# Kernel tuning notes

Hardware: AMD Instinct MI355X
Metric: run time of the kernel (lower is better)

Reference implementation:

```python
import jax, jax.numpy as jnp
import numpy as np

D_MODEL = 1024
N_HEADS = 16
K_TOP = 64
D_HEAD = D_MODEL // N_HEADS


def setup_inputs() -> dict:
    key = jax.random.key(0)
    ks = jax.random.split(key, 9)
    B, L = 8, 4096
    bound = 1.0 / np.sqrt(D_MODEL)  # nn.Linear default init range
    lin = lambda k: jax.random.uniform(k, (D_MODEL, D_MODEL), jnp.float32, -bound, bound)
    vec = lambda k: jax.random.uniform(k, (D_MODEL,), jnp.float32, -bound, bound)
    return {
        "query": jax.random.normal(ks[0], (B, L, D_MODEL), jnp.float32),
        "Wq": lin(ks[1]), "bq": vec(ks[2]),
        "Wk": lin(ks[3]), "bk": vec(ks[4]),
        "Wv": lin(ks[5]), "bv": vec(ks[6]),
        "Wo": lin(ks[7]), "bo": vec(ks[8]),
    }


def reference(query, Wq, bq, Wk, bk, Wv, bv, Wo, bo):
    B, L_q, D = query.shape
    L_k = L_q  # self-attention: key = value = query
    F_q = L_q // 2 + 1
    F_k = L_k // 2 + 1
    k_top = min(K_TOP, F_q)

    def proj(x, W, b):
        # (B, L, D) -> (B, H, L, d_head)
        return (x @ W + b).reshape(B, -1, N_HEADS, D_HEAD).transpose(0, 2, 1, 3)

    q = proj(query, Wq, bq)
    k = proj(query, Wk, bk)
    v = proj(query, Wv, bv)

    q_freq = jnp.fft.rfft(q, axis=2)  # (B, H, F_q, d_head) complex64
    k_freq = jnp.fft.rfft(k, axis=2)
    v_freq = jnp.fft.rfft(v, axis=2)

    # top-k frequency bins by mean spectral magnitude of the query
    q_energy = jnp.abs(q_freq).mean(axis=-1)  # (B, H, F_q)
    _, idx = jax.lax.top_k(q_energy, k_top)   # (B, H, k)
    mapped_idx = jnp.clip(
        jnp.round(idx.astype(jnp.float32) * (F_k - 1) / (F_q - 1)).astype(jnp.int32),
        0, F_k - 1)

    gather = lambda x, i: jnp.take_along_axis(x, i[..., None], axis=2)
    q_top = gather(q_freq, idx)          # (B, H, k, d_head)
    k_top_freq = gather(k_freq, mapped_idx)
    v_top = gather(v_freq, mapped_idx)

    eps = 1e-8
    attn_score = (q_top.real * k_top_freq.real).sum(-1) / (D_HEAD ** 0.5 + eps)
    attn = jax.nn.softmax(attn_score, axis=-1)[..., None]  # (B, H, k, 1)

    # fill spectrum with mean of query spectrum, then scatter attended bins
    q_mean_freq = q_freq.mean(axis=2, keepdims=True)  # (B, H, 1, d_head) complex
    out_freq = jnp.broadcast_to(q_mean_freq, (B, N_HEADS, F_q, D_HEAD))
    src = (attn * v_top.real).astype(out_freq.dtype)  # real -> complex (imag=0)
    bi = jnp.arange(B)[:, None, None]
    hi = jnp.arange(N_HEADS)[None, :, None]
    out_freq = out_freq.at[bi, hi, idx].set(src)

    out_time = jnp.fft.irfft(out_freq, n=L_q, axis=2)  # (B, H, L, d_head)
    out = out_time.transpose(0, 2, 1, 3).reshape(B, L_q, D)
    return out @ Wo + bo
```

## Files before the change

kernel.cpp:

```cpp
#include <hip/hip_runtime.h>
#include <math.h>
#include <stdint.h>


typedef _Float16 f16;
typedef _Float16 f16x8 __attribute__((ext_vector_type(8)));
typedef float f32x4 __attribute__((ext_vector_type(4)));

#define PI_F 3.14159265358979323846f
#define PADJ(j) ((j) + ((j) >> 3))

__device__ __forceinline__ void gl_lds16(const void* g, void* l) {
  __builtin_amdgcn_global_load_lds((const __attribute__((address_space(1))) void*)g,
                                   (__attribute__((address_space(3))) void*)l, 16, 0, 0);
}

__device__ __forceinline__ float2 cadd(float2 a, float2 b) { return make_float2(a.x + b.x, a.y + b.y); }
__device__ __forceinline__ float2 csub(float2 a, float2 b) { return make_float2(a.x - b.x, a.y - b.y); }
__device__ __forceinline__ float2 cmul(float2 a, float2 b) {
  return make_float2(a.x * b.x - a.y * b.y, a.x * b.y + a.y * b.x);
}
__device__ __forceinline__ float2 cmni(float2 a) { return make_float2(a.y, -a.x); }

__global__ __launch_bounds__(256) void k_tw(float2* __restrict__ twtab, float2* __restrict__ utab) {
  int j = blockIdx.x * 256 + threadIdx.x;
  if (j < 2048) {
    float ang = (float)j * (-6.28318530717958647692f / 2048.0f);
    twtab[j] = make_float2(cosf(ang), sinf(ang));
  } else if (j < 4097) {
    int f = j - 2048;
    float ang = (float)f * (-6.28318530717958647692f / 4096.0f);
    utab[f] = make_float2(cosf(ang), sinf(ang));
  }
}

__global__ __launch_bounds__(256) void k_prep(const float* __restrict__ Wq, const float* __restrict__ Wo,
                                              f16* __restrict__ WqT, f16* __restrict__ WoT) {
  __shared__ float t[32][33];
  const float* src = blockIdx.z ? Wo : Wq;
  f16* dst = blockIdx.z ? WoT : WqT;
  int c0 = blockIdx.x * 32, r0 = blockIdx.y * 32;
  int tx = threadIdx.x, ty = threadIdx.y;
#pragma unroll
  for (int yy = 0; yy < 4; ++yy)
    t[ty + yy * 8][tx] = src[(size_t)(r0 + ty + yy * 8) * 1024 + c0 + tx];
  __syncthreads();
#pragma unroll
  for (int yy = 0; yy < 4; ++yy)
    dst[(size_t)(c0 + ty + yy * 8) * 1024 + r0 + tx] = (f16)t[tx][ty + yy * 8];
}

__global__ __launch_bounds__(256) void k_prep2(const float* __restrict__ Wk, const float* __restrict__ Wv,
                                               f16* __restrict__ WkT, f16* __restrict__ WvT) {
  __shared__ float t[32][33];
  const float* src = blockIdx.z ? Wv : Wk;
  f16* dst = blockIdx.z ? WvT : WkT;
  int c0 = blockIdx.x * 32, r0 = blockIdx.y * 32;
  int tx = threadIdx.x, ty = threadIdx.y;
#pragma unroll
  for (int yy = 0; yy < 4; ++yy)
    t[ty + yy * 8][tx] = src[(size_t)(r0 + ty + yy * 8) * 1024 + c0 + tx];
  __syncthreads();
#pragma unroll
  for (int yy = 0; yy < 4; ++yy)
    dst[(size_t)(c0 + ty + yy * 8) * 1024 + r0 + tx] = (f16)t[tx][ty + yy * 8];
}

__global__ __launch_bounds__(256) void k_t1(const float* __restrict__ X, float* __restrict__ Xt) {
  __shared__ float t[32][33];
  int b = blockIdx.z;
  int l0 = blockIdx.x * 32, d0 = blockIdx.y * 32;
  int tx = threadIdx.x, ty = threadIdx.y;
#pragma unroll
  for (int yy = 0; yy < 4; ++yy)
    t[ty + yy * 8][tx] = X[((size_t)b * 4096 + l0 + ty + yy * 8) * 1024 + d0 + tx];
  __syncthreads();
#pragma unroll
  for (int yy = 0; yy < 4; ++yy)
    Xt[((size_t)b * 1024 + d0 + ty + yy * 8) * 4096 + l0 + tx] = t[tx][ty + yy * 8];
}

__device__ __forceinline__ void r8_stage(const float2* __restrict__ cur, float2* __restrict__ nxt,
                                         const float2* __restrict__ tw, int tid, int lg) {
  int Ls = 1 << lg;
  int p = tid >> lg, q = tid & (Ls - 1);
  float2 x[8];
#pragma unroll
  for (int u = 0; u < 8; ++u) x[u] = cur[PADJ(tid + 256 * u)];
  float2 s0 = cadd(x[0], x[4]), d0v = csub(x[0], x[4]);
  float2 s1 = cadd(x[2], x[6]), d1v = csub(x[2], x[6]);
  float2 e0 = cadd(s0, s1), e2 = csub(s0, s1);
  float2 md1 = cmni(d1v);
  float2 e1 = cadd(d0v, md1), e3 = csub(d0v, md1);
  float2 t0 = cadd(x[1], x[5]), u0 = csub(x[1], x[5]);
  float2 t1 = cadd(x[3], x[7]), u1 = csub(x[3], x[7]);
  float2 o0 = cadd(t0, t1), o2 = csub(t0, t1);
  float2 mu1 = cmni(u1);
  float2 o1 = cadd(u0, mu1), o3 = csub(u0, mu1);
  const float C8 = 0.70710678118654752440f;
  float2 w1 = make_float2(C8 * (o1.x + o1.y), C8 * (o1.y - o1.x));
  float2 w2 = cmni(o2);
  float2 w3 = make_float2(C8 * (o3.y - o3.x), -C8 * (o3.x + o3.y));
  float2 y[8];
  y[0] = cadd(e0, o0); y[4] = csub(e0, o0);
  y[1] = cadd(e1, w1); y[5] = csub(e1, w1);
  y[2] = cadd(e2, w2); y[6] = csub(e2, w2);
  y[3] = cadd(e3, w3); y[7] = csub(e3, w3);
  int tb = p << lg;
#pragma unroll
  for (int v = 1; v < 8; ++v) y[v] = cmul(y[v], tw[tb * v]);
  int ob = q + (p << (lg + 3));
#pragma unroll
  for (int v = 0; v < 8; ++v) nxt[PADJ(ob + (v << lg))] = y[v];
}

__global__ __launch_bounds__(256) void k_fft(const float* __restrict__ Xt,
                                             const float2* __restrict__ twtab,
                                             const float2* __restrict__ utab,
                                             f16* __restrict__ PReU, f16* __restrict__ PImU,
                                             float* __restrict__ sumXf) {
  __shared__ float2 bufA[2304];
  __shared__ float2 bufB[2304];
  __shared__ float redr[256], redi[256];
  int tid = threadIdx.x;
  int blk = blockIdx.x;

  const float4* src = (const float4*)(Xt + (size_t)blk * 4096);
#pragma unroll
  for (int r = 0; r < 4; ++r) {
    int i4 = r * 256 + tid;
    float4 v = src[i4];
    bufA[PADJ(2 * i4)] = make_float2(v.x, v.y);
    bufA[PADJ(2 * i4 + 1)] = make_float2(v.z, v.w);
  }
  __syncthreads();
  r8_stage(bufA, bufB, twtab, tid, 0);
  __syncthreads();
  r8_stage(bufB, bufA, twtab, tid, 3);
  __syncthreads();
  r8_stage(bufA, bufB, twtab, tid, 6);
  __syncthreads();
#pragma unroll
  for (int h = 0; h < 2; ++h) {
    int i = (h << 8) + tid;
    float2 a0 = bufB[PADJ(i)], a1 = bufB[PADJ(i + 512)];
    float2 a2 = bufB[PADJ(i + 1024)], a3 = bufB[PADJ(i + 1536)];
    float2 s02 = cadd(a0, a2), d02 = csub(a0, a2);
    float2 s13 = cadd(a1, a3), d13m = cmni(csub(a1, a3));
    bufA[PADJ(i)] = cadd(s02, s13);
    bufA[PADJ(i + 512)] = cadd(d02, d13m);
    bufA[PADJ(i + 1024)] = csub(s02, s13);
    bufA[PADJ(i + 1536)] = csub(d02, d13m);
  }
  __syncthreads();
  float sumr = 0.f, sumi = 0.f;
  size_t obase = (size_t)blk * 2049;
  for (int f = tid; f <= 2048; f += 256) {
    int fz = f & 2047, fm = (2048 - f) & 2047;
    float2 z = bufA[PADJ(fz)], m = bufA[PADJ(fm)];
    float Er = 0.5f * (z.x + m.x), Ei = 0.5f * (z.y - m.y);
    float Or = 0.5f * (z.y + m.y), Oi = -0.5f * (z.x - m.x);
    float2 wv = utab[f];
    float Xr = Er + wv.x * Or - wv.y * Oi;
    float Xi = Ei + wv.x * Oi + wv.y * Or;
    PReU[obase + f] = (f16)Xr;
    PImU[obase + f] = (f16)Xi;
    sumr += Xr; sumi += Xi;
  }
  __syncthreads();
  redr[tid] = sumr; redi[tid] = sumi;
  __syncthreads();
  for (int s = 128; s > 0; s >>= 1) {
    if (tid < s) { redr[tid] += redr[tid + s]; redi[tid] += redi[tid + s]; }
    __syncthreads();
  }
  if (tid == 0) { sumXf[2 * blk] = redr[0]; sumXf[2 * blk + 1] = redi[0]; }
}

__global__ __launch_bounds__(256) void k_C(const float* __restrict__ sumXf, const float* __restrict__ Wq,
                                           const float* __restrict__ bq,
                                           float* __restrict__ Cre, float* __restrict__ Cim) {
  int b = blockIdx.x >> 2;
  int hd = ((blockIdx.x & 3) << 8) + threadIdx.x;
  float accr = 0.f, acci = 0.f;
  for (int dm = 0; dm < 1024; ++dm) {
    float w = Wq[(size_t)dm * 1024 + hd];
    accr += sumXf[2 * (b * 1024 + dm)] * w;
    acci += sumXf[2 * (b * 1024 + dm) + 1] * w;
  }
  Cre[b * 1024 + hd] = (accr + 4096.0f * bq[hd]) * (1.0f / 2049.0f);
  Cim[b * 1024 + hd] = acci * (1.0f / 2049.0f);
}

__global__ __launch_bounds__(256) void k_t2(const f16* __restrict__ PReU, const f16* __restrict__ PImU,
                                            f16* __restrict__ PT) {
  __shared__ f16 t[32][33];
  int z = blockIdx.z;
  int b = z >> 1, pl = z & 1;
  const f16* src = pl ? PImU : PReU;
  int f0 = blockIdx.x * 32, d0 = blockIdx.y * 32;
  int tx = threadIdx.x, ty = threadIdx.y;
#pragma unroll
  for (int yy = 0; yy < 4; ++yy) {
    int ff = f0 + tx;
    t[ty + yy * 8][tx] = (ff < 2049) ? src[(size_t)(b * 1024 + d0 + ty + yy * 8) * 2049 + ff] : (f16)0.f;
  }
  __syncthreads();
#pragma unroll
  for (int yy = 0; yy < 4; ++yy)
    PT[((size_t)b * 4352 + 2 * (f0 + ty + yy * 8) + pl) * 1024 + d0 + tx] = t[tx][ty + yy * 8];
}

__global__ __launch_bounds__(256) void k_energy(const f16* __restrict__ PT, const f16* __restrict__ WqT,
                                                const float* __restrict__ bq, float* __restrict__ energy) {
  __shared__ __align__(16) f16 sA[128 * 64];
  __shared__ __align__(16) f16 sB[128 * 64];
  int tid = threadIdx.x;
  int lane = tid & 63, w = tid >> 6;
  int lin = blockIdx.x;
  int xq = lin & 7, rq = lin >> 3;
  int bN = rq & 7;
  int Mblk = ((rq >> 3) << 3) + xq;
  int wr = w >> 1, wc = w & 1;
  f32x4 acc[4][4];
#pragma unroll
  for (int mf = 0; mf < 4; ++mf)
#pragma unroll
    for (int nf = 0; nf < 4; ++nf) acc[mf][nf] = 0;

  const char* gA0 = (const char*)PT + (size_t)(Mblk * 128) * 2048;
  const char* gB0 = (const char*)WqT + (size_t)(bN * 128) * 2048;
  int swz = ((tid & 7) ^ ((tid >> 3) & 7)) << 4;
  int r = lane & 15;
  int cq = (lane >> 4) << 4;

  for (int ks = 0; ks < 16; ++ks) {
    int kb = ks * 128;
#pragma unroll
    for (int it = 0; it < 4; ++it) {
      int row = it * 32 + (tid >> 3);
      gl_lds16(gA0 + (size_t)row * 2048 + kb + swz, (char*)sA + it * 4096 + w * 1024);
    }
#pragma unroll
    for (int it = 0; it < 4; ++it) {
      int row = it * 32 + (tid >> 3);
      gl_lds16(gB0 + (size_t)row * 2048 + kb + swz, (char*)sB + it * 4096 + w * 1024);
    }
    __syncthreads();
#pragma unroll
    for (int kk = 0; kk < 64; kk += 32) {
      int cb = (kk << 1) + cq;
      f16x8 aF[4], bF[4];
#pragma unroll
      for (int mf = 0; mf < 4; ++mf) {
        int row = wr * 64 + mf * 16 + r;
        aF[mf] = *(const f16x8*)((const char*)sA + row * 128 + (cb ^ ((row & 7) << 4)));
      }
#pragma unroll
      for (int nf = 0; nf < 4; ++nf) {
        int row = wc * 64 + nf * 16 + r;
        bF[nf] = *(const f16x8*)((const char*)sB + row * 128 + (cb ^ ((row & 7) << 4)));
      }
#pragma unroll
      for (int mf = 0; mf < 4; ++mf)
#pragma unroll
        for (int nf = 0; nf < 4; ++nf)
          acc[mf][nf] = __builtin_amdgcn_mfma_f32_16x16x32_f16(aF[mf], bF[nf], acc[mf][nf], 0, 0, 0);
    }
    __syncthreads();
  }
  int b = Mblk / 34;
  int tIb = Mblk - b * 34;
  int head = 2 * bN + wc;
  int q = lane >> 4;
  bool dc = (tIb == 0 && wr == 0 && q == 0);
#pragma unroll
  for (int mf = 0; mf < 4; ++mf) {
    float sE = 0.f, sO = 0.f;
#pragma unroll
    for (int nf = 0; nf < 4; ++nf) {
      float re0 = acc[mf][nf][0], im0 = acc[mf][nf][1];
      float re1 = acc[mf][nf][2], im1 = acc[mf][nf][3];
      if (dc && mf == 0) re0 += 4096.0f * bq[head * 64 + nf * 16 + r];
      sE += sqrtf(re0 * re0 + im0 * im0);
      sO += sqrtf(re1 * re1 + im1 * im1);
    }
#pragma unroll
    for (int off = 1; off < 16; off <<= 1) {
      sE += __shfl_xor(sE, off);
      sO += __shfl_xor(sO, off);
    }
    if (r == 0) {
      int fp = tIb * 64 + wr * 32 + mf * 8 + (q << 1);
      energy[((size_t)b * 16 + head) * 2176 + fp] = sE * 0.015625f;
      energy[((size_t)b * 16 + head) * 2176 + fp + 1] = sO * 0.015625f;
    }
  }
}

__global__ __launch_bounds__(256) void k_topk(const float* __restrict__ energy, int* __restrict__ idxb) {
  __shared__ float vals[2049];
  __shared__ unsigned long long wbest[4];
  int tid = threadIdx.x, bh = blockIdx.x;
  const float* e = energy + (size_t)bh * 2176;
  for (int i = tid; i < 2049; i += 256) vals[i] = e[i];
  __syncthreads();
  for (int it = 0; it < 64; ++it) {
    unsigned long long best = 0ull;
    for (int f = tid; f < 2049; f += 256) {
      unsigned b32 = __float_as_uint(vals[f]);
      b32 = (b32 & 0x80000000u) ? ~b32 : (b32 | 0x80000000u);
      unsigned long long k = ((unsigned long long)b32 << 12) | (unsigned)(4095 - f);
      best = (k > best) ? k : best;
    }
#pragma unroll
    for (int off = 32; off > 0; off >>= 1) {
      unsigned long long o = __shfl_xor(best, off);
      best = (o > best) ? o : best;
    }
    if ((tid & 63) == 0) wbest[tid >> 6] = best;
    __syncthreads();
    if (tid == 0) {
      unsigned long long b0 = wbest[0] > wbest[1] ? wbest[0] : wbest[1];
      unsigned long long b1 = wbest[2] > wbest[3] ? wbest[2] : wbest[3];
      unsigned long long bb = b0 > b1 ? b0 : b1;
      int f = 4095 - (int)(bb & 4095ull);
      idxb[bh * 64 + it] = f;
      vals[f] = -1.0f;
    }
    __syncthreads();
  }
}

__global__ __launch_bounds__(256) void k_qkv(const f16* __restrict__ PT, const int* __restrict__ idxb,
                                             const f16* __restrict__ WqT, const f16* __restrict__ WkT,
                                             const f16* __restrict__ WvT, float* __restrict__ part) {
  __shared__ __align__(16) f16 sA[64 * 64];
  __shared__ __align__(16) f16 sB[192 * 64];
  __shared__ int fjs[64];
  int tid = threadIdx.x, lane = tid & 63, w = tid >> 6;
  int bh = blockIdx.x, ks = blockIdx.y;
  int b = bh >> 4, h = bh & 15;
  if (tid < 64) fjs[tid] = idxb[bh * 64 + tid];
  __syncthreads();
  f32x4 acc[4][3];
#pragma unroll
  for (int mf = 0; mf < 4; ++mf)
#pragma unroll
    for (int nf = 0; nf < 3; ++nf) acc[mf][nf] = 0;

  int l8 = lane & 7;
  int lr = lane >> 3;
  int swz = (l8 ^ lr) << 4;

  for (int kt = 0; kt < 4; ++kt) {
    int kbyte = ks * 512 + kt * 128;
#pragma unroll
    for (int t = 0; t < 2; ++t) {
      int ia = w * 2 + t;
      int row = ia * 8 + lr;
      const char* src = (const char*)PT + (size_t)(b * 4352 + 2 * fjs[row]) * 2048 + kbyte + swz;
      gl_lds16(src, (char*)sA + ia * 1024);
    }
#pragma unroll
    for (int t = 0; t < 6; ++t) {
      int ib = w * 6 + t;
      int row = ib * 8 + lr;
      const f16* Wt = (row < 64) ? WqT : (row < 128) ? WkT : WvT;
      const char* src = (const char*)Wt + (size_t)(h * 64 + (row & 63)) * 2048 + kbyte + swz;
      gl_lds16(src, (char*)sB + ib * 1024);
    }
    __syncthreads();
#pragma unroll
    for (int kk = 0; kk < 64; kk += 32) {
      int cb = (kk << 1) + ((lane >> 4) << 4);
      int r = lane & 15;
      f16x8 aF[4], bF[3];
#pragma unroll
      for (int mf = 0; mf < 4; ++mf) {
        int row = mf * 16 + r;
        aF[mf] = *(const f16x8*)((const char*)sA + row * 128 + (cb ^ ((row & 7) << 4)));
      }
#pragma unroll
      for (int nf = 0; nf < 3; ++nf) {
        int row = w * 48 + nf * 16 + r;
        bF[nf] = *(const f16x8*)((const char*)sB + row * 128 + (cb ^ ((row & 7) << 4)));
      }
#pragma unroll
      for (int mf = 0; mf < 4; ++mf)
#pragma unroll
        for (int nf = 0; nf < 3; ++nf)
          acc[mf][nf] = __builtin_amdgcn_mfma_f32_16x16x32_f16(aF[mf], bF[nf], acc[mf][nf], 0, 0, 0);
    }
    __syncthreads();
  }
  float* pb = part + (size_t)(ks * 128 + bh) * 12288;
#pragma unroll
  for (int mf = 0; mf < 4; ++mf)
#pragma unroll
    for (int nf = 0; nf < 3; ++nf)
#pragma unroll
      for (int rr = 0; rr < 4; ++rr) {
        int m = mf * 16 + ((lane >> 4) << 2) + rr;
        int n = w * 48 + nf * 16 + (lane & 15);
        pb[m * 192 + n] = acc[mf][nf][rr];
      }
}

__global__ __launch_bounds__(256) void k_attn2(const float* __restrict__ part, const int* __restrict__ idxb,
                                               const float* __restrict__ bq, const float* __restrict__ bk,
                                               const float* __restrict__ bv, const float* __restrict__ Cre,
                                               float* __restrict__ amp) {
  __shared__ float sQKV[64][196];
  __shared__ float scores[64], attns[64];
  __shared__ int fjs[64];
  __shared__ int dcrow;
  int tid = threadIdx.x, bh = blockIdx.x;
  int b = bh >> 4, h = bh & 15;
  if (tid == 0) dcrow = -1;
  __syncthreads();
  if (tid < 64) {
    int f = idxb[bh * 64 + tid];
    fjs[tid] = f;
    if (f == 0) dcrow = tid;
  }
  __syncthreads();
  const float4* p0 = (const float4*)(part + (size_t)bh * 12288);
  const size_t s4 = (size_t)128 * 12288 / 4;
#pragma unroll
  for (int it = 0; it < 12; ++it) {
    int e = it * 256 + tid;
    float4 v0 = p0[e], v1 = p0[e + s4], v2 = p0[e + 2 * s4], v3 = p0[e + 3 * s4];
    float4 v;
    v.x = v0.x + v1.x + v2.x + v3.x;
    v.y = v0.y + v1.y + v2.y + v3.y;
    v.z = v0.z + v1.z + v2.z + v3.z;
    v.w = v0.w + v1.w + v2.w + v3.w;
    int m = e / 48, n0 = (e % 48) * 4;
    *(float4*)&sQKV[m][n0] = v;
  }
  __syncthreads();
  if (dcrow >= 0 && tid < 192) {
    const float* bias = (tid < 64) ? bq : (tid < 128) ? bk : bv;
    sQKV[dcrow][tid] += 4096.0f * bias[h * 64 + (tid & 63)];
  }
  __syncthreads();
  {
    int j = tid >> 2, p = tid & 3;
    float s = 0.f;
#pragma unroll
    for (int c = 0; c < 16; ++c) {
      int cc = p * 16 + c;
      s = fmaf(sQKV[j][cc], sQKV[j][64 + cc], s);
    }
    s += __shfl_xor(s, 1);
    s += __shfl_xor(s, 2);
    if (p == 0) scores[j] = s * 0.125f;
  }
  __syncthreads();
  if (tid < 64) {
    float s = scores[tid];
    float m = s;
#pragma unroll
    for (int off = 32; off > 0; off >>= 1) m = fmaxf(m, __shfl_xor(m, off));
    float ev = expf(s - m);
    float sm = ev;
#pragma unroll
    for (int off = 32; off > 0; off >>= 1) sm += __shfl_xor(sm, off);
    attns[tid] = ev / sm;
  }
  __syncthreads();
  {
    int j = tid >> 2, d0 = (tid & 3) * 16;
    float at = attns[j];
    int fj = fjs[j];
    float wj = (fj == 0 || fj == 2048) ? 0.5f : 1.0f;
    float* ao = amp + ((size_t)bh * 64 + j) * 64 + d0;
#pragma unroll
    for (int q4 = 0; q4 < 4; ++q4) {
      float4 c4 = *(const float4*)&Cre[b * 1024 + h * 64 + d0 + q4 * 4];
      float4 vv = *(const float4*)&sQKV[j][128 + d0 + q4 * 4];
      float4 av;
      av.x = wj * (at * vv.x - c4.x);
      av.y = wj * (at * vv.y - c4.y);
      av.z = wj * (at * vv.z - c4.z);
      av.w = wj * (at * vv.w - c4.w);
      *(float4*)&ao[q4 * 4] = av;
    }
  }
}

__global__ __launch_bounds__(256) void k_ot(const float* __restrict__ amp, const int* __restrict__ idxb,
                                            const float* __restrict__ Cre, const float* __restrict__ Cim,
                                            f16* __restrict__ OT) {
  __shared__ __align__(16) float sAmp[64][64];
  __shared__ __align__(16) float sCre[64];
  __shared__ __align__(16) float sCim[64];
  __shared__ int fjs[64];
  int tid = threadIdx.x;
  int bh = blockIdx.x >> 4, tch = blockIdx.x & 15;
  int b = bh >> 4, h = bh & 15;
  for (int e = tid; e < 4096; e += 256) ((float*)sAmp)[e] = amp[(size_t)bh * 4096 + e];
  if (tid < 64) {
    sCre[tid] = Cre[b * 1024 + h * 64 + tid];
    sCim[tid] = Cim[b * 1024 + h * 64 + tid];
    fjs[tid] = idxb[bh * 64 + tid];
  }
  __syncthreads();
  int t = tch * 256 + tid;
  float4 acc[16];
#pragma unroll
  for (int d4 = 0; d4 < 16; ++d4) acc[d4] = make_float4(0.f, 0.f, 0.f, 0.f);
  float ssum = 0.f;
  for (int jj = 0; jj < 64; ++jj) {
    int r = (fjs[jj] * t) & 4095;
    float ang = (float)r * 0.00153398078788564123f;
    float sn, cs;
    __sincosf(ang, &sn, &cs);
    ssum += sn;
    const float4* arow = (const float4*)&sAmp[jj][0];
#pragma unroll
    for (int d4 = 0; d4 < 16; ++d4) {
      float4 a = arow[d4];
      acc[d4].x = fmaf(a.x, cs, acc[d4].x);
      acc[d4].y = fmaf(a.y, cs, acc[d4].y);
      acc[d4].z = fmaf(a.z, cs, acc[d4].z);
      acc[d4].w = fmaf(a.w, cs, acc[d4].w);
    }
  }
  float g = ssum;
  if (t & 1) {
    int tp = (t <= 2048) ? t : 4096 - t;
    float sg = (t <= 2048) ? 1.f : -1.f;
    float aa = (float)tp * (PI_F / 4096.0f);
    g -= sg * (cosf(aa) / sinf(aa));
  }
  const float s2L = 2.0f / 4096.0f;
  int isT0 = (t == 0);
  f16* o16 = OT + ((size_t)bh * 4096 + t) * 64;
#pragma unroll
  for (int d4 = 0; d4 < 16; ++d4) {
    float4 ci4 = *(const float4*)&sCim[d4 * 4];
    float4 cr4 = *(const float4*)&sCre[d4 * 4];
    acc[d4].x = s2L * (acc[d4].x + ci4.x * g) + (isT0 ? cr4.x : 0.f);
    acc[d4].y = s2L * (acc[d4].y + ci4.y * g) + (isT0 ? cr4.y : 0.f);
    acc[d4].z = s2L * (acc[d4].z + ci4.z * g) + (isT0 ? cr4.z : 0.f);
    acc[d4].w = s2L * (acc[d4].w + ci4.w * g) + (isT0 ? cr4.w : 0.f);
  }
#pragma unroll
  for (int p = 0; p < 8; ++p) {
    float4 a = acc[2 * p], bb = acc[2 * p + 1];
    f16x8 v;
    v[0] = (f16)a.x; v[1] = (f16)a.y; v[2] = (f16)a.z; v[3] = (f16)a.w;
    v[4] = (f16)bb.x; v[5] = (f16)bb.y; v[6] = (f16)bb.z; v[7] = (f16)bb.w;
    *(f16x8*)(o16 + p * 8) = v;
  }
}

__global__ __launch_bounds__(256) void k_final(const f16* __restrict__ OT, const f16* __restrict__ WoT,
                                               const float* __restrict__ bo, float* __restrict__ out) {
  __shared__ __align__(16) f16 sA[128 * 64];
  __shared__ __align__(16) f16 sB[128 * 64];
  int tid = threadIdx.x, lane = tid & 63, wv = tid >> 6;
  int lin = blockIdx.x;
  int xq = lin & 7, rq = lin >> 3;
  int bN = rq & 7;
  int Mblk = ((rq >> 3) << 3) + xq;
  int wr = wv >> 1, wc = wv & 1;
  f32x4 acc[4][4];
#pragma unroll
  for (int mf = 0; mf < 4; ++mf)
#pragma unroll
    for (int nf = 0; nf < 4; ++nf) acc[mf][nf] = 0;
  int b = Mblk >> 5, t0 = (Mblk & 31) * 128;
  const char* gB0 = (const char*)WoT + (size_t)(bN * 128) * 2048;
  int swz = ((tid & 7) ^ ((tid >> 3) & 7)) << 4;
  int r = lane & 15;
  int cq = (lane >> 4) << 4;
  for (int ks = 0; ks < 16; ++ks) {
    const char* gA = (const char*)OT + (size_t)((b * 16 + ks) * 4096 + t0) * 128;
#pragma unroll
    for (int it = 0; it < 4; ++it) {
      int row = it * 32 + (tid >> 3);
      gl_lds16(gA + (size_t)row * 128 + swz, (char*)sA + it * 4096 + wv * 1024);
    }
    int kb = ks * 128;
#pragma unroll
    for (int it = 0; it < 4; ++it) {
      int row = it * 32 + (tid >> 3);
      gl_lds16(gB0 + (size_t)row * 2048 + kb + swz, (char*)sB + it * 4096 + wv * 1024);
    }
    __syncthreads();
#pragma unroll
    for (int kk = 0; kk < 64; kk += 32) {
      int cb = (kk << 1) + cq;
      f16x8 aF[4], bF[4];
#pragma unroll
      for (int mf = 0; mf < 4; ++mf) {
        int row = wr * 64 + mf * 16 + r;
        aF[mf] = *(const f16x8*)((const char*)sA + row * 128 + (cb ^ ((row & 7) << 4)));
      }
#pragma unroll
      for (int nf = 0; nf < 4; ++nf) {
        int row = wc * 64 + nf * 16 + r;
        bF[nf] = *(const f16x8*)((const char*)sB + row * 128 + (cb ^ ((row & 7) << 4)));
      }
#pragma unroll
      for (int mf = 0; mf < 4; ++mf)
#pragma unroll
        for (int nf = 0; nf < 4; ++nf)
          acc[mf][nf] = __builtin_amdgcn_mfma_f32_16x16x32_f16(aF[mf], bF[nf], acc[mf][nf], 0, 0, 0);
    }
    __syncthreads();
  }
#pragma unroll
  for (int nf = 0; nf < 4; ++nf) {
    int gcol = bN * 128 + wc * 64 + nf * 16 + (lane & 15);
    float bcol = bo[gcol];
#pragma unroll
    for (int mf = 0; mf < 4; ++mf) {
#pragma unroll
      for (int rr = 0; rr < 4; ++rr) {
        int grow = Mblk * 128 + wr * 64 + mf * 16 + ((lane >> 4) << 2) + rr;
        out[(size_t)grow * 1024 + gcol] = acc[mf][nf][rr] + bcol;
      }
    }
  }
}

extern "C" void kernel_launch(void* const* d_in, const int* in_sizes, int n_in,
                              void* d_out, int out_size, void* d_ws, size_t ws_size,
                              hipStream_t stream) {
  const float* X = (const float*)d_in[0];
  const float* Wq = (const float*)d_in[1];
  const float* bq = (const float*)d_in[2];
  const float* Wk = (const float*)d_in[3];
  const float* bk = (const float*)d_in[4];
  const float* Wv = (const float*)d_in[5];
  const float* bv = (const float*)d_in[6];
  const float* Wo = (const float*)d_in[7];
  const float* bo = (const float*)d_in[8];
  float* out = (float*)d_out;

  if (ws_size < 208928768ULL) return;
  char* w = (char*)d_ws;
  float* Xt = (float*)(w);
  f16* PT = (f16*)(w);
  f16* WkT = (f16*)(w + 71303168);
  f16* WvT = (f16*)(w + 73400320);
  float* part = (float*)(w + 75497472);
  char* R2 = w + 134217728;
  f16* PReU = (f16*)(R2);
  f16* PImU = (f16*)(R2 + 33570816);
  f16* OT = (f16*)(R2);
  char* R3 = R2 + 67141632;
  float* sumXf = (float*)(R3);
  float* Cre = (float*)(R3 + 65536);
  float* Cim = (float*)(R3 + 98304);
  float* energy = (float*)(R3 + 131072);
  int* idxb = (int*)(R3 + 1245184);
  float* amp = (float*)(R3 + 1277952);
  f16* WqT = (f16*)(R3 + 3375104);
  f16* WoT = (f16*)(R3 + 5472256);
  float2* twtab = (float2*)d_out;
  float2* utab = twtab + 2048;

  dim3 b32(32, 8);
  hipLaunchKernelGGL(k_tw, dim3(17), dim3(256), 0, stream, twtab, utab);
  hipLaunchKernelGGL(k_prep, dim3(32, 32, 2), b32, 0, stream, Wq, Wo, WqT, WoT);
  hipLaunchKernelGGL(k_t1, dim3(128, 32, 8), b32, 0, stream, X, Xt);
  hipLaunchKernelGGL(k_fft, dim3(8192), dim3(256), 0, stream, Xt, twtab, utab, PReU, PImU, sumXf);
  hipLaunchKernelGGL(k_prep2, dim3(32, 32, 2), b32, 0, stream, Wk, Wv, WkT, WvT);
  hipLaunchKernelGGL(k_C, dim3(32), dim3(256), 0, stream, sumXf, Wq, bq, Cre, Cim);
  hipLaunchKernelGGL(k_t2, dim3(68, 32, 16), b32, 0, stream, PReU, PImU, PT);
  hipLaunchKernelGGL(k_energy, dim3(2176), dim3(256), 0, stream, PT, WqT, bq, energy);
  hipLaunchKernelGGL(k_topk, dim3(128), dim3(256), 0, stream, energy, idxb);
  hipLaunchKernelGGL(k_qkv, dim3(128, 4), dim3(256), 0, stream, PT, idxb, WqT, WkT, WvT, part);
  hipLaunchKernelGGL(k_attn2, dim3(128), dim3(256), 0, stream, part, idxb, bq, bk, bv, Cre, amp);
  hipLaunchKernelGGL(k_ot, dim3(2048), dim3(256), 0, stream, amp, idxb, Cre, Cim, OT);
  hipLaunchKernelGGL(k_final, dim3(2048), dim3(256), 0, stream, OT, WoT, bo, out);
}
```

Before: 584.9 us.

## Enlarge GEMM tiles to 256x256 with double-buffered LDS in energy and final GEMMs

Rewrites the two big MFMA GEMM kernels (energy and output projection) to use 512-thread blocks with 256x256 output tiles and double-buffered LDS staging. The next K slice is prefetched with global_load_lds while the current one is computed, using manual vmcnt waits and barriers. The aim is to hide global-load latency and raise arithmetic intensity per block. In exchange it uses 128KB of LDS per block, more accumulator registers, and fewer blocks, which could cut occupancy or cause tail imbalance.

```diff
diff --git a/kernel.cpp b/kernel.cpp
--- a/kernel.cpp
+++ b/kernel.cpp
@@ -21,6 +21,14 @@
   return make_float2(a.x * b.x - a.y * b.y, a.x * b.y + a.y * b.x);
 }
 __device__ __forceinline__ float2 cmni(float2 a) { return make_float2(a.y, -a.x); }
+
+__device__ __forceinline__ void stage4(const char* g, size_t stride, char* lds, int tid, int w, int swz) {
+#pragma unroll
+  for (int it = 0; it < 4; ++it) {
+    int row = it * 64 + (tid >> 3);
+    gl_lds16(g + (size_t)row * stride + swz, lds + it * 8192 + w * 1024);
+  }
+}
 
 __global__ __launch_bounds__(256) void k_tw(float2* __restrict__ twtab, float2* __restrict__ utab) {
   int j = blockIdx.x * 256 + threadIdx.x;
@@ -211,77 +219,73 @@
     PT[((size_t)b * 4352 + 2 * (f0 + ty + yy * 8) + pl) * 1024 + d0 + tx] = t[tx][ty + yy * 8];
 }
 
-__global__ __launch_bounds__(256) void k_energy(const f16* __restrict__ PT, const f16* __restrict__ WqT,
-                                                const float* __restrict__ bq, float* __restrict__ energy) {
-  __shared__ __align__(16) f16 sA[128 * 64];
-  __shared__ __align__(16) f16 sB[128 * 64];
-  int tid = threadIdx.x;
-  int lane = tid & 63, w = tid >> 6;
-  int lin = blockIdx.x;
-  int xq = lin & 7, rq = lin >> 3;
-  int bN = rq & 7;
-  int Mblk = ((rq >> 3) << 3) + xq;
-  int wr = w >> 1, wc = w & 1;
-  f32x4 acc[4][4];
-#pragma unroll
-  for (int mf = 0; mf < 4; ++mf)
+__global__ __launch_bounds__(512, 2) void k_energy(const f16* __restrict__ PT, const f16* __restrict__ WqT,
+                                                   const float* __restrict__ bq, float* __restrict__ energy) {
+  __shared__ __align__(16) f16 sA[2][256 * 64];
+  __shared__ __align__(16) f16 sB[2][256 * 64];
+  int tid = threadIdx.x, lane = tid & 63, w = tid >> 6;
+  int wm = w >> 2, wn = w & 3;
+  int sw = (blockIdx.x & 7) * 68 + (blockIdx.x >> 3);
+  int bN = sw & 3, Mblk = sw >> 2;
+  int swz = ((tid & 7) ^ ((tid >> 3) & 7)) << 4;
+  int r = lane & 15, q = lane >> 4;
+  int cq = q << 4;
+  f32x4 acc[8][4];
+#pragma unroll
+  for (int mf = 0; mf < 8; ++mf)
 #pragma unroll
     for (int nf = 0; nf < 4; ++nf) acc[mf][nf] = 0;
 
-  const char* gA0 = (const char*)PT + (size_t)(Mblk * 128) * 2048;
-  const char* gB0 = (const char*)WqT + (size_t)(bN * 128) * 2048;
-  int swz = ((tid & 7) ^ ((tid >> 3) & 7)) << 4;
-  int r = lane & 15;
-  int cq = (lane >> 4) << 4;
-
+  const char* gA0 = (const char*)PT + (size_t)(Mblk * 256) * 2048;
+  const char* gB0 = (const char*)WqT + (size_t)(bN * 256) * 2048;
+
+  stage4(gA0, 2048, (char*)sA[0], tid, w, swz);
+  stage4(gB0, 2048, (char*)sB[0], tid, w, swz);
   for (int ks = 0; ks < 16; ++ks) {
-    int kb = ks * 128;
-#pragma unroll
-    for (int it = 0; it < 4; ++it) {
-      int row = it * 32 + (tid >> 3);
-      gl_lds16(gA0 + (size_t)row * 2048 + kb + swz, (char*)sA + it * 4096 + w * 1024);
-    }
-#pragma unroll
-    for (int it = 0; it < 4; ++it) {
-      int row = it * 32 + (tid >> 3);
-      gl_lds16(gB0 + (size_t)row * 2048 + kb + swz, (char*)sB + it * 4096 + w * 1024);
-    }
-    __syncthreads();
+    int cur = ks & 1;
+    if (ks < 15) {
+      int kb = (ks + 1) * 128;
+      stage4(gA0 + kb, 2048, (char*)sA[cur ^ 1], tid, w, swz);
+      stage4(gB0 + kb, 2048, (char*)sB[cur ^ 1], tid, w, swz);
+      asm volatile("s_waitcnt vmcnt(8)\ns_barrier" ::: "memory");
+    } else {
+      asm volatile("s_waitcnt vmcnt(0)\ns_barrier" ::: "memory");
+    }
+    const char* bA = (const char*)sA[cur];
+    const char* bB = (const char*)sB[cur];
 #pragma unroll
     for (int kk = 0; kk < 64; kk += 32) {
       int cb = (kk << 1) + cq;
-      f16x8 aF[4], bF[4];
-#pragma unroll
-      for (int mf = 0; mf < 4; ++mf) {
-        int row = wr * 64 + mf * 16 + r;
-        aF[mf] = *(const f16x8*)((const char*)sA + row * 128 + (cb ^ ((row & 7) << 4)));
+      f16x8 aF[8], bF[4];
+#pragma unroll
+      for (int mf = 0; mf < 8; ++mf) {
+        int row = wm * 128 + mf * 16 + r;
+        aF[mf] = *(const f16x8*)(bA + row * 128 + (cb ^ ((row & 7) << 4)));
       }
 #pragma unroll
       for (int nf = 0; nf < 4; ++nf) {
-        int row = wc * 64 + nf * 16 + r;
-        bF[nf] = *(const f16x8*)((const char*)sB + row * 128 + (cb ^ ((row & 7) << 4)));
-      }
-#pragma unroll
-      for (int mf = 0; mf < 4; ++mf)
+        int row = wn * 64 + nf * 16 + r;
+        bF[nf] = *(const f16x8*)(bB + row * 128 + (cb ^ ((row & 7) << 4)));
+      }
+#pragma unroll
+      for (int mf = 0; mf < 8; ++mf)
 #pragma unroll
         for (int nf = 0; nf < 4; ++nf)
           acc[mf][nf] = __builtin_amdgcn_mfma_f32_16x16x32_f16(aF[mf], bF[nf], acc[mf][nf], 0, 0, 0);
     }
-    __syncthreads();
-  }
-  int b = Mblk / 34;
-  int tIb = Mblk - b * 34;
-  int head = 2 * bN + wc;
-  int q = lane >> 4;
-  bool dc = (tIb == 0 && wr == 0 && q == 0);
-#pragma unroll
-  for (int mf = 0; mf < 4; ++mf) {
+    asm volatile("s_barrier" ::: "memory");
+  }
+  int bb = Mblk / 17, tIb = Mblk - bb * 17;
+  int hd = bN * 4 + wn;
+  bool dc = (tIb == 0 && wm == 0 && q == 0);
+#pragma unroll
+  for (int mf = 0; mf < 8; ++mf) {
     float sE = 0.f, sO = 0.f;
 #pragma unroll
     for (int nf = 0; nf < 4; ++nf) {
       float re0 = acc[mf][nf][0], im0 = acc[mf][nf][1];
       float re1 = acc[mf][nf][2], im1 = acc[mf][nf][3];
-      if (dc && mf == 0) re0 += 4096.0f * bq[head * 64 + nf * 16 + r];
+      if (dc && mf == 0) re0 += 4096.0f * bq[hd * 64 + nf * 16 + r];
       sE += sqrtf(re0 * re0 + im0 * im0);
       sO += sqrtf(re1 * re1 + im1 * im1);
     }
@@ -291,9 +295,9 @@
       sO += __shfl_xor(sO, off);
     }
     if (r == 0) {
-      int fp = tIb * 64 + wr * 32 + mf * 8 + (q << 1);
-      energy[((size_t)b * 16 + head) * 2176 + fp] = sE * 0.015625f;
-      energy[((size_t)b * 16 + head) * 2176 + fp + 1] = sO * 0.015625f;
+      int fp = tIb * 128 + wm * 64 + mf * 8 + (q << 1);
+      energy[((size_t)bb * 16 + hd) * 2176 + fp] = sE * 0.015625f;
+      energy[((size_t)bb * 16 + hd) * 2176 + fp + 1] = sO * 0.015625f;
     }
   }
 }
@@ -557,72 +561,72 @@
   }
 }
 
-__global__ __launch_bounds__(256) void k_final(const f16* __restrict__ OT, const f16* __restrict__ WoT,
-                                               const float* __restrict__ bo, float* __restrict__ out) {
-  __shared__ __align__(16) f16 sA[128 * 64];
-  __shared__ __align__(16) f16 sB[128 * 64];
-  int tid = threadIdx.x, lane = tid & 63, wv = tid >> 6;
-  int lin = blockIdx.x;
-  int xq = lin & 7, rq = lin >> 3;
-  int bN = rq & 7;
-  int Mblk = ((rq >> 3) << 3) + xq;
-  int wr = wv >> 1, wc = wv & 1;
-  f32x4 acc[4][4];
-#pragma unroll
-  for (int mf = 0; mf < 4; ++mf)
+__global__ __launch_bounds__(512, 2) void k_final(const f16* __restrict__ OT, const f16* __restrict__ WoT,
+                                                  const float* __restrict__ bo, float* __restrict__ out) {
+  __shared__ __align__(16) f16 sA[2][256 * 64];
+  __shared__ __align__(16) f16 sB[2][256 * 64];
+  int tid = threadIdx.x, lane = tid & 63, w = tid >> 6;
+  int wm = w >> 2, wn = w & 3;
+  int sw = (blockIdx.x & 7) * 64 + (blockIdx.x >> 3);
+  int bN = sw & 3, Mblk = sw >> 2;
+  int swz = ((tid & 7) ^ ((tid >> 3) & 7)) << 4;
+  int r = lane & 15, q = lane >> 4;
+  int cq = q << 4;
+  f32x4 acc[8][4];
+#pragma unroll
+  for (int mf = 0; mf < 8; ++mf)
 #pragma unroll
     for (int nf = 0; nf < 4; ++nf) acc[mf][nf] = 0;
-  int b = Mblk >> 5, t0 = (Mblk & 31) * 128;
-  const char* gB0 = (const char*)WoT + (size_t)(bN * 128) * 2048;
-  int swz = ((tid & 7) ^ ((tid >> 3) & 7)) << 4;
-  int r = lane & 15;
-  int cq = (lane >> 4) << 4;
+
+  int b = Mblk >> 4, t0 = (Mblk & 15) * 256;
+  const char* gAb = (const char*)OT + ((size_t)(b * 16) * 4096 + t0) * 128;
+  const char* gB0 = (const char*)WoT + (size_t)(bN * 256) * 2048;
+
+  stage4(gAb, 128, (char*)sA[0], tid, w, swz);
+  stage4(gB0, 2048, (char*)sB[0], tid, w, swz);
   for (int ks = 0; ks < 16; ++ks) {
-    const char* gA = (const char*)OT + (size_t)((b * 16 + ks) * 4096 + t0) * 128;
-#pragma unroll
-    for (int it = 0; it < 4; ++it) {
-      int row = it * 32 + (tid >> 3);
-      gl_lds16(gA + (size_t)row * 128 + swz, (char*)sA + it * 4096 + wv * 1024);
-    }
-    int kb = ks * 128;
-#pragma unroll
-    for (int it = 0; it < 4; ++it) {
-      int row = it * 32 + (tid >> 3);
-      gl_lds16(gB0 + (size_t)row * 2048 + kb + swz, (char*)sB + it * 4096 + wv * 1024);
-    }
-    __syncthreads();
+    int cur = ks & 1;
+    if (ks < 15) {
+      stage4(gAb + (size_t)(ks + 1) * 4096 * 128, 128, (char*)sA[cur ^ 1], tid, w, swz);
+      stage4(gB0 + (ks + 1) * 128, 2048, (char*)sB[cur ^ 1], tid, w, swz);
+      asm volatile("s_waitcnt vmcnt(8)\ns_barrier" ::: "memory");
+    } else {
+      asm volatile("s_waitcnt vmcnt(0)\ns_barrier" ::: "memory");
+    }
+    const char* bA = (const char*)sA[cur];
+    const char* bB = (const char*)sB[cur];
 #pragma unroll
     for (int kk = 0; kk < 64; kk += 32) {
       int cb = (kk << 1) + cq;
-      f16x8 aF[4], bF[4];
-#pragma unroll
-      for (int mf = 0; mf < 4; ++mf) {
-        int row = wr * 64 + mf * 16 + r;
-        aF[mf] = *(const f16x8*)((const char*)sA + row * 128 + (cb ^ ((row & 7) << 4)));
+      f16x8 aF[8], bF[4];
+#pragma unroll
+      for (int mf = 0; mf < 8; ++mf) {
+        int row = wm * 128 + mf * 16 + r;
+        aF[mf] = *(const f16x8*)(bA + row * 128 + (cb ^ ((row & 7) << 4)));
       }
 #pragma unroll
       for (int nf = 0; nf < 4; ++nf) {
-        int row = wc * 64 + nf * 16 + r;
-        bF[nf] = *(const f16x8*)((const char*)sB + row * 128 + (cb ^ ((row & 7) << 4)));
-      }
-#pragma unroll
-      for (int mf = 0; mf < 4; ++mf)
+        int row = wn * 64 + nf * 16 + r;
+        bF[nf] = *(const f16x8*)(bB + row * 128 + (cb ^ ((row & 7) << 4)));
+      }
+#pragma unroll
+      for (int mf = 0; mf < 8; ++mf)
 #pragma unroll
         for (int nf = 0; nf < 4; ++nf)
           acc[mf][nf] = __builtin_amdgcn_mfma_f32_16x16x32_f16(aF[mf], bF[nf], acc[mf][nf], 0, 0, 0);
     }
-    __syncthreads();
+    asm volatile("s_barrier" ::: "memory");
   }
 #pragma unroll
   for (int nf = 0; nf < 4; ++nf) {
-    int gcol = bN * 128 + wc * 64 + nf * 16 + (lane & 15);
+    int gcol = bN * 256 + wn * 64 + nf * 16 + r;
     float bcol = bo[gcol];
 #pragma unroll
-    for (int mf = 0; mf < 4; ++mf) {
-#pragma unroll
-      for (int rr = 0; rr < 4; ++rr) {
-        int grow = Mblk * 128 + wr * 64 + mf * 16 + ((lane >> 4) << 2) + rr;
-        out[(size_t)grow * 1024 + gcol] = acc[mf][nf][rr] + bcol;
+    for (int mf = 0; mf < 8; ++mf) {
+#pragma unroll
+      for (int e = 0; e < 4; ++e) {
+        int grow = Mblk * 256 + wm * 128 + mf * 16 + (q << 2) + e;
+        out[(size_t)grow * 1024 + gcol] = acc[mf][nf][e] + bcol;
       }
     }
   }
@@ -673,10 +677,10 @@
   hipLaunchKernelGGL(k_prep2, dim3(32, 32, 2), b32, 0, stream, Wk, Wv, WkT, WvT);
   hipLaunchKernelGGL(k_C, dim3(32), dim3(256), 0, stream, sumXf, Wq, bq, Cre, Cim);
   hipLaunchKernelGGL(k_t2, dim3(68, 32, 16), b32, 0, stream, PReU, PImU, PT);
-  hipLaunchKernelGGL(k_energy, dim3(2176), dim3(256), 0, stream, PT, WqT, bq, energy);
+  hipLaunchKernelGGL(k_energy, dim3(544), dim3(512), 0, stream, PT, WqT, bq, energy);
   hipLaunchKernelGGL(k_topk, dim3(128), dim3(256), 0, stream, energy, idxb);
   hipLaunchKernelGGL(k_qkv, dim3(128, 4), dim3(256), 0, stream, PT, idxb, WqT, WkT, WvT, part);
   hipLaunchKernelGGL(k_attn2, dim3(128), dim3(256), 0, stream, part, idxb, bq, bk, bv, Cre, amp);
   hipLaunchKernelGGL(k_ot, dim3(2048), dim3(256), 0, stream, amp, idxb, Cre, Cim, OT);
-  hipLaunchKernelGGL(k_final, dim3(2048), dim3(256), 0, stream, OT, WoT, bo, out);
-}
+  hipLaunchKernelGGL(k_final, dim3(512), dim3(512), 0, stream, OT, WoT, bo, out);
+}
```

Result: no change. 593.1 us (+1.4%).

## Double-buffer LDS staging in energy and output-projection GEMMs

Applied to the files above, without the earlier changes.

Converts the k_energy and k_final GEMM main loops to double-buffered LDS, issuing global-to-LDS loads for the next K tile before computing on the current one. It uses explicit s_waitcnt vmcnt(8) plus s_barrier so only the older tile's loads must finish. The aim is to hide global memory latency behind MFMA work. The cost is doubled LDS (64KB per block), and launch bounds are set for 2 blocks per CU. The hand-written waitcnt relies on the exact count of outstanding loads.

```diff
diff --git a/kernel.cpp b/kernel.cpp
--- a/kernel.cpp
+++ b/kernel.cpp
@@ -21,6 +21,15 @@
   return make_float2(a.x * b.x - a.y * b.y, a.x * b.y + a.y * b.x);
 }
 __device__ __forceinline__ float2 cmni(float2 a) { return make_float2(a.y, -a.x); }
+
+__device__ __forceinline__ void stg4(const char* g, size_t stride, int kb, char* lds,
+                                     int tid, int w, int swz) {
+#pragma unroll
+  for (int it = 0; it < 4; ++it) {
+    int row = it * 32 + (tid >> 3);
+    gl_lds16(g + (size_t)row * stride + kb + swz, lds + it * 4096 + w * 1024);
+  }
+}
 
 __global__ __launch_bounds__(256) void k_tw(float2* __restrict__ twtab, float2* __restrict__ utab) {
   int j = blockIdx.x * 256 + threadIdx.x;
@@ -211,10 +220,10 @@
     PT[((size_t)b * 4352 + 2 * (f0 + ty + yy * 8) + pl) * 1024 + d0 + tx] = t[tx][ty + yy * 8];
 }
 
-__global__ __launch_bounds__(256) void k_energy(const f16* __restrict__ PT, const f16* __restrict__ WqT,
-                                                const float* __restrict__ bq, float* __restrict__ energy) {
-  __shared__ __align__(16) f16 sA[128 * 64];
-  __shared__ __align__(16) f16 sB[128 * 64];
+__global__ __launch_bounds__(256, 2) void k_energy(const f16* __restrict__ PT, const f16* __restrict__ WqT,
+                                                   const float* __restrict__ bq, float* __restrict__ energy) {
+  __shared__ __align__(16) f16 sA[2][128 * 64];
+  __shared__ __align__(16) f16 sB[2][128 * 64];
   int tid = threadIdx.x;
   int lane = tid & 63, w = tid >> 6;
   int lin = blockIdx.x;
@@ -231,22 +240,23 @@
   const char* gA0 = (const char*)PT + (size_t)(Mblk * 128) * 2048;
   const char* gB0 = (const char*)WqT + (size_t)(bN * 128) * 2048;
   int swz = ((tid & 7) ^ ((tid >> 3) & 7)) << 4;
-  int r = lane & 15;
-  int cq = (lane >> 4) << 4;
-
+  int r = lane & 15, q = lane >> 4;
+  int cq = q << 4;
+
+  stg4(gA0, 2048, 0, (char*)&sA[0][0], tid, w, swz);
+  stg4(gB0, 2048, 0, (char*)&sB[0][0], tid, w, swz);
   for (int ks = 0; ks < 16; ++ks) {
-    int kb = ks * 128;
-#pragma unroll
-    for (int it = 0; it < 4; ++it) {
-      int row = it * 32 + (tid >> 3);
-      gl_lds16(gA0 + (size_t)row * 2048 + kb + swz, (char*)sA + it * 4096 + w * 1024);
-    }
-#pragma unroll
-    for (int it = 0; it < 4; ++it) {
-      int row = it * 32 + (tid >> 3);
-      gl_lds16(gB0 + (size_t)row * 2048 + kb + swz, (char*)sB + it * 4096 + w * 1024);
-    }
-    __syncthreads();
+    int cur = ks & 1;
+    if (ks < 15) {
+      int kb = (ks + 1) * 128;
+      stg4(gA0, 2048, kb, (char*)&sA[cur ^ 1][0], tid, w, swz);
+      stg4(gB0, 2048, kb, (char*)&sB[cur ^ 1][0], tid, w, swz);
+      asm volatile("s_waitcnt vmcnt(8)\ns_barrier" ::: "memory");
+    } else {
+      asm volatile("s_waitcnt vmcnt(0)\ns_barrier" ::: "memory");
+    }
+    const char* bA = (const char*)&sA[cur][0];
+    const char* bB = (const char*)&sB[cur][0];
 #pragma unroll
     for (int kk = 0; kk < 64; kk += 32) {
       int cb = (kk << 1) + cq;
@@ -254,12 +264,12 @@
 #pragma unroll
       for (int mf = 0; mf < 4; ++mf) {
         int row = wr * 64 + mf * 16 + r;
-        aF[mf] = *(const f16x8*)((const char*)sA + row * 128 + (cb ^ ((row & 7) << 4)));
+        aF[mf] = *(const f16x8*)(bA + row * 128 + (cb ^ ((row & 7) << 4)));
       }
 #pragma unroll
       for (int nf = 0; nf < 4; ++nf) {
         int row = wc * 64 + nf * 16 + r;
-        bF[nf] = *(const f16x8*)((const char*)sB + row * 128 + (cb ^ ((row & 7) << 4)));
+        bF[nf] = *(const f16x8*)(bB + row * 128 + (cb ^ ((row & 7) << 4)));
       }
 #pragma unroll
       for (int mf = 0; mf < 4; ++mf)
@@ -267,12 +277,11 @@
         for (int nf = 0; nf < 4; ++nf)
           acc[mf][nf] = __builtin_amdgcn_mfma_f32_16x16x32_f16(aF[mf], bF[nf], acc[mf][nf], 0, 0, 0);
     }
-    __syncthreads();
+    asm volatile("s_barrier" ::: "memory");
   }
   int b = Mblk / 34;
   int tIb = Mblk - b * 34;
   int head = 2 * bN + wc;
-  int q = lane >> 4;
   bool dc = (tIb == 0 && wr == 0 && q == 0);
 #pragma unroll
   for (int mf = 0; mf < 4; ++mf) {
@@ -557,10 +566,10 @@
   }
 }
 
-__global__ __launch_bounds__(256) void k_final(const f16* __restrict__ OT, const f16* __restrict__ WoT,
-                                               const float* __restrict__ bo, float* __restrict__ out) {
-  __shared__ __align__(16) f16 sA[128 * 64];
-  __shared__ __align__(16) f16 sB[128 * 64];
+__global__ __launch_bounds__(256, 2) void k_final(const f16* __restrict__ OT, const f16* __restrict__ WoT,
+                                                  const float* __restrict__ bo, float* __restrict__ out) {
+  __shared__ __align__(16) f16 sA[2][128 * 64];
+  __shared__ __align__(16) f16 sB[2][128 * 64];
   int tid = threadIdx.x, lane = tid & 63, wv = tid >> 6;
   int lin = blockIdx.x;
   int xq = lin & 7, rq = lin >> 3;
@@ -575,22 +584,23 @@
   int b = Mblk >> 5, t0 = (Mblk & 31) * 128;
   const char* gB0 = (const char*)WoT + (size_t)(bN * 128) * 2048;
   int swz = ((tid & 7) ^ ((tid >> 3) & 7)) << 4;
-  int r = lane & 15;
-  int cq = (lane >> 4) << 4;
+  int r = lane & 15, q = lane >> 4;
+  int cq = q << 4;
+#define GA_TILE(ks) ((const char*)OT + (size_t)((b * 16 + (ks)) * 4096 + t0) * 128)
+
+  stg4(GA_TILE(0), 128, 0, (char*)&sA[0][0], tid, wv, swz);
+  stg4(gB0, 2048, 0, (char*)&sB[0][0], tid, wv, swz);
   for (int ks = 0; ks < 16; ++ks) {
-    const char* gA = (const char*)OT + (size_t)((b * 16 + ks) * 4096 + t0) * 128;
-#pragma unroll
-    for (int it = 0; it < 4; ++it) {
-      int row = it * 32 + (tid >> 3);
-      gl_lds16(gA + (size_t)row * 128 + swz, (char*)sA + it * 4096 + wv * 1024);
-    }
-    int kb = ks * 128;
-#pragma unroll
-    for (int it = 0; it < 4; ++it) {
-      int row = it * 32 + (tid >> 3);
-      gl_lds16(gB0 + (size_t)row * 2048 + kb + swz, (char*)sB + it * 4096 + wv * 1024);
-    }
-    __syncthreads();
+    int cur = ks & 1;
+    if (ks < 15) {
+      stg4(GA_TILE(ks + 1), 128, 0, (char*)&sA[cur ^ 1][0], tid, wv, swz);
+      stg4(gB0, 2048, (ks + 1) * 128, (char*)&sB[cur ^ 1][0], tid, wv, swz);
+      asm volatile("s_waitcnt vmcnt(8)\ns_barrier" ::: "memory");
+    } else {
+      asm volatile("s_waitcnt vmcnt(0)\ns_barrier" ::: "memory");
+    }
+    const char* bA = (const char*)&sA[cur][0];
+    const char* bB = (const char*)&sB[cur][0];
 #pragma unroll
     for (int kk = 0; kk < 64; kk += 32) {
       int cb = (kk << 1) + cq;
@@ -598,12 +608,12 @@
 #pragma unroll
       for (int mf = 0; mf < 4; ++mf) {
         int row = wr * 64 + mf * 16 + r;
-        aF[mf] = *(const f16x8*)((const char*)sA + row * 128 + (cb ^ ((row & 7) << 4)));
+        aF[mf] = *(const f16x8*)(bA + row * 128 + (cb ^ ((row & 7) << 4)));
       }
 #pragma unroll
       for (int nf = 0; nf < 4; ++nf) {
         int row = wc * 64 + nf * 16 + r;
-        bF[nf] = *(const f16x8*)((const char*)sB + row * 128 + (cb ^ ((row & 7) << 4)));
+        bF[nf] = *(const f16x8*)(bB + row * 128 + (cb ^ ((row & 7) << 4)));
       }
 #pragma unroll
       for (int mf = 0; mf < 4; ++mf)
@@ -611,17 +621,18 @@
         for (int nf = 0; nf < 4; ++nf)
           acc[mf][nf] = __builtin_amdgcn_mfma_f32_16x16x32_f16(aF[mf], bF[nf], acc[mf][nf], 0, 0, 0);
     }
-    __syncthreads();
-  }
+    asm volatile("s_barrier" ::: "memory");
+  }
+#undef GA_TILE
 #pragma unroll
   for (int nf = 0; nf < 4; ++nf) {
-    int gcol = bN * 128 + wc * 64 + nf * 16 + (lane & 15);
+    int gcol = bN * 128 + wc * 64 + nf * 16 + r;
     float bcol = bo[gcol];
 #pragma unroll
     for (int mf = 0; mf < 4; ++mf) {
 #pragma unroll
       for (int rr = 0; rr < 4; ++rr) {
-        int grow = Mblk * 128 + wr * 64 + mf * 16 + ((lane >> 4) << 2) + rr;
+        int grow = Mblk * 128 + wr * 64 + mf * 16 + (q << 2) + rr;
         out[(size_t)grow * 1024 + gcol] = acc[mf][nf][rr] + bcol;
       }
     }
```

Measured after the change: 573.7 us. About the same (-1.9%).
